# Kernel optimization log

Measured on AMD Instinct MI355X. Metric: run time of the kernel, lower is better.

Reference implementation:

```python
import jax, jax.numpy as jnp
import numpy as np

VOCAB = 100000
EMB = 256
HID = 512
HH = HID // 2  # per-direction hidden
NTAGS = 12
START = 10
STOP = 11
SEQ = 2048
NEG = -10000.0


def setup_inputs() -> dict:
    key = jax.random.key(0)
    ks = jax.random.split(key, 18)
    s = 0.05
    inp = {
        "sentence": jax.random.randint(ks[0], (SEQ,), 0, VOCAB, dtype=jnp.int64 if jax.config.jax_enable_x64 else jnp.int32),
        "tags": jax.random.randint(ks[1], (SEQ,), 0, 10, dtype=jnp.int64 if jax.config.jax_enable_x64 else jnp.int32),
        "embed": jax.random.normal(ks[2], (VOCAB, EMB), jnp.float32) * s,
        "Wih_f": jax.random.normal(ks[3], (4 * HH, EMB), jnp.float32) * s,
        "Whh_f": jax.random.normal(ks[4], (4 * HH, HH), jnp.float32) * s,
        "bih_f": jax.random.normal(ks[5], (4 * HH,), jnp.float32) * s,
        "bhh_f": jax.random.normal(ks[6], (4 * HH,), jnp.float32) * s,
        "Wih_b": jax.random.normal(ks[7], (4 * HH, EMB), jnp.float32) * s,
        "Whh_b": jax.random.normal(ks[8], (4 * HH, HH), jnp.float32) * s,
        "bih_b": jax.random.normal(ks[9], (4 * HH,), jnp.float32) * s,
        "bhh_b": jax.random.normal(ks[10], (4 * HH,), jnp.float32) * s,
        "W_out": jax.random.normal(ks[11], (NTAGS, HID), jnp.float32) * s,
        "b_out": jax.random.normal(ks[12], (NTAGS,), jnp.float32) * s,
        "h0": jax.random.normal(ks[14], (2, HH), jnp.float32),
        "c0": jax.random.normal(ks[15], (2, HH), jnp.float32),
    }
    trans = jax.random.normal(ks[13], (NTAGS, NTAGS), jnp.float32)
    trans = trans.at[START, :].set(NEG)  # never transition INTO start
    trans = trans.at[:, STOP].set(NEG)   # never transition FROM stop
    inp["transitions"] = trans
    return inp


def _lstm_dir(x, h0, c0, Wih, Whh, bih, bhh):
    # x: [T, E]; PyTorch gate order i, f, g, o
    pre = x @ Wih.T + bih + bhh  # [T, 4*HH] precomputed input projection
    def step(carry, p):
        h, c = carry
        g = p + Whh @ h
        i, f, gg, o = jnp.split(g, 4)
        i = jax.nn.sigmoid(i)
        f = jax.nn.sigmoid(f)
        gg = jnp.tanh(gg)
        o = jax.nn.sigmoid(o)
        c = f * c + i * gg
        h = o * jnp.tanh(c)
        return (h, c), h
    _, hs = jax.lax.scan(step, (h0, c0), pre)
    return hs  # [T, HH]


def _forward_impl(sentence, tags, embed, Wih_f, Whh_f, bih_f, bhh_f,
                  Wih_b, Whh_b, bih_b, bhh_b, W_out, b_out, transitions, h0, c0):
    x = embed[sentence]  # [T, E]
    hf = _lstm_dir(x, h0[0], c0[0], Wih_f, Whh_f, bih_f, bhh_f)
    hb = jnp.flip(_lstm_dir(jnp.flip(x, 0), h0[1], c0[1], Wih_b, Whh_b, bih_b, bhh_b), 0)
    feats = jnp.concatenate([hf, hb], axis=-1) @ W_out.T + b_out  # [T, NTAGS]

    # CRF forward algorithm: log-semiring scan over time
    fv0 = jnp.full((NTAGS,), NEG, feats.dtype).at[START].set(0.0)
    def crf_step(fv, emit):
        # transitions[next, prev]; logsumexp over prev
        fv = jax.nn.logsumexp(fv[None, :] + transitions + emit[:, None], axis=1)
        return fv, None
    fv, _ = jax.lax.scan(crf_step, fv0, feats)
    forward_score = jax.nn.logsumexp(fv + transitions[STOP])

    # gold path score
    prev = jnp.concatenate([jnp.array([START], dtype=tags.dtype), tags[:-1]])
    emit_gold = jnp.take_along_axis(feats, tags[:, None], axis=1)[:, 0]
    gold_score = jnp.sum(transitions[tags, prev]) + jnp.sum(emit_gold) + transitions[STOP, tags[-1]]

    return forward_score - gold_score


def reference(sentence, tags, embed, Wih_f, Whh_f, bih_f, bhh_f,
              Wih_b, Whh_b, bih_b, bhh_b, W_out, b_out, transitions, h0, c0):
    return _forward_impl(sentence, tags, embed, Wih_f, Whh_f, bih_f, bhh_f,
                         Wih_b, Whh_b, bih_b, bhh_b, W_out, b_out, transitions, h0, c0)
```

## Files before the change

kernel.cpp:

```cpp
#include <hip/hip_runtime.h>
#include <hip/hip_bf16.h>
#include <stdint.h>

#define SEQ   2048
#define EMB   256
#define HHD   256
#define GATES 1024
#define NTAGS 12
#define START 10
#define STOP  11
#define CCH   16
#define CLEN  128

__device__ __forceinline__ int sdot4(uint32_t a, uint32_t b, int c) {
#if __has_builtin(__builtin_amdgcn_sdot4)
  return __builtin_amdgcn_sdot4((int)a, (int)b, c, false);
#else
  int r = c;
#pragma unroll
  for (int i = 0; i < 4; i++) {
    int av = (int)(signed char)((a >> (8 * i)) & 255);
    int bv = (int)(signed char)((b >> (8 * i)) & 255);
    r += av * bv;
  }
  return r;
#endif
}

__device__ __forceinline__ float fsig(float x) {
  float e = __expf(-x);
  return __builtin_amdgcn_rcpf(1.0f + e);
}

__device__ __forceinline__ int dpp_xor1(int x) {
  return __builtin_amdgcn_update_dpp(0, x, 0xB1, 0xF, 0xF, true);
}
__device__ __forceinline__ int dpp_xor2(int x) {
  return __builtin_amdgcn_update_dpp(0, x, 0x4E, 0xF, 0xF, true);
}
__device__ __forceinline__ float dpp_xor2_f(float x) {
  int r = __builtin_amdgcn_update_dpp(0, __float_as_int(x), 0x4E, 0xF, 0xF, true);
  return __int_as_float(r);
}

__global__ __launch_bounds__(256) void k_front(const float* __restrict__ whh_f,
                                               const float* __restrict__ whh_b,
                                               uint32_t* __restrict__ q4,
                                               float* __restrict__ scales,
                                               const int* __restrict__ sentence,
                                               const float* __restrict__ embed,
                                               const float* __restrict__ Wih_f,
                                               const float* __restrict__ bih_f,
                                               const float* __restrict__ bhh_f,
                                               const float* __restrict__ Wih_b,
                                               const float* __restrict__ bih_b,
                                               const float* __restrict__ bhh_b,
                                               float* __restrict__ pre) {
  if (blockIdx.x < 512) {
    const int row  = (blockIdx.x * 256 + threadIdx.x) >> 6;
    const int lane = threadIdx.x & 63;
    const int d = row >> 10, r = row & 1023;
    const float4 w = *(const float4*)((d ? whh_b : whh_f) + (long)r * HHD + lane * 4);
    float m = fmaxf(fmaxf(fabsf(w.x), fabsf(w.y)), fmaxf(fabsf(w.z), fabsf(w.w)));
#pragma unroll
    for (int off = 32; off; off >>= 1) m = fmaxf(m, __shfl_xor(m, off, 64));
    m = fmaxf(m, 1e-20f);
    const float inv = 127.f / m;
    int a = (int)rintf(w.x * inv), b = (int)rintf(w.y * inv);
    int c = (int)rintf(w.z * inv), e = (int)rintf(w.w * inv);
    q4[row * 64 + lane] = (uint32_t)(a & 255) | ((uint32_t)(b & 255) << 8) |
                          ((uint32_t)(c & 255) << 16) | ((uint32_t)(e & 255) << 24);
    if (lane == 0) scales[row] = m / 127.f;
    return;
  }
  const int bid2 = blockIdx.x - 512;
  const int dir  = bid2 >> 8;
  const int t0   = (bid2 & 255) * 8;
  const float* Wih = dir ? Wih_b : Wih_f;
  const float* bih = dir ? bih_b : bih_f;
  const float* bhh = dir ? bhh_b : bhh_f;

  __shared__ float xs[8][256];
  const int uu = threadIdx.x;
#pragma unroll
  for (int i = 0; i < 8; i++) {
    int s = sentence[t0 + i];
    xs[i][uu] = embed[(long)s * EMB + uu];
  }
  __syncthreads();

  float acc[4][8];
#pragma unroll
  for (int j = 0; j < 4; j++)
#pragma unroll
    for (int t = 0; t < 8; t++) acc[j][t] = 0.f;

  const float4* W4 = (const float4*)Wih;
  for (int kq = 0; kq < 64; kq++) {
    float4 w[4];
#pragma unroll
    for (int j = 0; j < 4; j++) w[j] = W4[(j * 256 + uu) * 64 + kq];
#pragma unroll
    for (int t = 0; t < 8; t++) {
      float4 xv = ((const float4*)xs[t])[kq];
#pragma unroll
      for (int j = 0; j < 4; j++)
        acc[j][t] += w[j].x * xv.x + w[j].y * xv.y + w[j].z * xv.z + w[j].w * xv.w;
    }
  }
  float bs[4];
#pragma unroll
  for (int j = 0; j < 4; j++) bs[j] = bih[j * 256 + uu] + bhh[j * 256 + uu];
#pragma unroll
  for (int t = 0; t < 8; t++) {
    float4 o = {acc[0][t] + bs[0], acc[1][t] + bs[1],
                acc[2][t] + bs[2], acc[3][t] + bs[3]};
    *(float4*)&pre[(((long)(dir * SEQ + t0 + t)) * HHD + uu) * 4] = o;
  }
}

__global__ __launch_bounds__(512, 2) void k_lstm(const uint32_t* __restrict__ q4,
                                                 const float* __restrict__ scales,
                                                 const float* __restrict__ pre,
                                                 const float* __restrict__ h0,
                                                 const float* __restrict__ c0,
                                                 float* __restrict__ hs) {
  const int dir  = blockIdx.x;
  const int L    = threadIdx.x;
  const int q    = L & 3;
  const int g    = L >> 2;
  const int p    = q & 1;
  const int half = q >> 1;
  const int u    = 2 * g + p;

  __shared__ __align__(16) uint8_t hbuf[2][256];

  const long base = (long)dir * GATES;

  uint4 wa[4][4], wb[4][4];
  const uint4* qq = (const uint4*)q4;
#pragma unroll
  for (int j = 0; j < 4; j++) {
    const int qj = q ^ j;
    const int rA = (2 * (qj >> 1)) * 256 + 2 * g + (qj & 1);
    const int rB = rA + 256;
#pragma unroll
    for (int k = 0; k < 4; k++) {
      wa[j][k] = qq[(base + rA) * 16 + 4 * q + k];
      wb[j][k] = qq[(base + rB) * 16 + 4 * q + k];
    }
  }
  const int rown = (2 * half) * 256 + u;
  const float sA = scales[base + rown];
  const float sB = scales[base + rown + 256];

  if (L < 256) {
    float v = h0[dir * HHD + L] * (127.f / 4.f);
    v = fminf(fmaxf(v, -127.f), 127.f);
    hbuf[0][L] = (uint8_t)(int)rintf(v);
  }
  float c_st = c0[dir * HHD + u];
  __syncthreads();

  const int t0 = dir ? (SEQ - 1) : 0;
  const long pstep = dir ? -(long)(HHD * 4) : (long)(HHD * 4);
  const long hstep = dir ? -(long)HHD : (long)HHD;
  const float* pp = pre + (long)dir * SEQ * (HHD * 4) + ((long)t0 * HHD + u) * 4 + 2 * half;
  float* hp       = hs  + (long)dir * SEQ * HHD + (long)t0 * HHD + u;
  const float gmul = half ? 2.f : 1.f;
  const int write_h = ((L & 2) == 0);

  for (int s = 0; s < SEQ; s++) {
    const float2 pr = *(const float2*)pp;

    const uint4* hq4 = (const uint4*)(hbuf[s & 1] + (q << 6));
    const uint4 h0v = hq4[0], h1v = hq4[1], h2v = hq4[2], h3v = hq4[3];

    int pa0 = 0, pa1 = 0, pa2 = 0, pa3 = 0;
    int pb0 = 0, pb1 = 0, pb2 = 0, pb3 = 0;
#pragma unroll
    for (int k = 0; k < 4; k++) {
      const uint4 hk = (k == 0) ? h0v : (k == 1) ? h1v : (k == 2) ? h2v : h3v;
      pa0 = sdot4(wa[0][k].x, hk.x, pa0); pa0 = sdot4(wa[0][k].y, hk.y, pa0);
      pa0 = sdot4(wa[0][k].z, hk.z, pa0); pa0 = sdot4(wa[0][k].w, hk.w, pa0);
      pa1 = sdot4(wa[1][k].x, hk.x, pa1); pa1 = sdot4(wa[1][k].y, hk.y, pa1);
      pa1 = sdot4(wa[1][k].z, hk.z, pa1); pa1 = sdot4(wa[1][k].w, hk.w, pa1);
      pa2 = sdot4(wa[2][k].x, hk.x, pa2); pa2 = sdot4(wa[2][k].y, hk.y, pa2);
      pa2 = sdot4(wa[2][k].z, hk.z, pa2); pa2 = sdot4(wa[2][k].w, hk.w, pa2);
      pa3 = sdot4(wa[3][k].x, hk.x, pa3); pa3 = sdot4(wa[3][k].y, hk.y, pa3);
      pa3 = sdot4(wa[3][k].z, hk.z, pa3); pa3 = sdot4(wa[3][k].w, hk.w, pa3);
      pb0 = sdot4(wb[0][k].x, hk.x, pb0); pb0 = sdot4(wb[0][k].y, hk.y, pb0);
      pb0 = sdot4(wb[0][k].z, hk.z, pb0); pb0 = sdot4(wb[0][k].w, hk.w, pb0);
      pb1 = sdot4(wb[1][k].x, hk.x, pb1); pb1 = sdot4(wb[1][k].y, hk.y, pb1);
      pb1 = sdot4(wb[1][k].z, hk.z, pb1); pb1 = sdot4(wb[1][k].w, hk.w, pb1);
      pb2 = sdot4(wb[2][k].x, hk.x, pb2); pb2 = sdot4(wb[2][k].y, hk.y, pb2);
      pb2 = sdot4(wb[2][k].z, hk.z, pb2); pb2 = sdot4(wb[2][k].w, hk.w, pb2);
      pb3 = sdot4(wb[3][k].x, hk.x, pb3); pb3 = sdot4(wb[3][k].y, hk.y, pb3);
      pb3 = sdot4(wb[3][k].z, hk.z, pb3); pb3 = sdot4(wb[3][k].w, hk.w, pb3);
    }
    const int tA = pa0 + dpp_xor1(pa1);
    const int tA2 = pa2 + dpp_xor1(pa3);
    const int sumA = tA + dpp_xor2(tA2);
    const int tB = pb0 + dpp_xor1(pb1);
    const int tB2 = pb2 + dpp_xor1(pb3);
    const int sumB = tB + dpp_xor2(tB2);

    const float hsc = (s == 0) ? (4.f / 127.f) : (1.f / 127.f);
    const float gA = pr.x + sA * hsc * (float)sumA;
    const float gB = pr.y + sB * hsc * (float)sumB;

    const float v0 = fsig(gA * gmul) * gmul - (gmul - 1.f);
    const float v1 = fsig(gB);
    const float p0 = dpp_xor2_f(v0);
    const float p1 = dpp_xor2_f(v1);
    const float iv = half ? p0 : v0;
    const float fv = half ? p1 : v1;
    const float gv = half ? v0 : p0;
    const float ov = half ? v1 : p1;

    c_st = fv * c_st + iv * gv;
    const float hv = ov * (2.f * fsig(2.f * c_st) - 1.f);

    if (write_h) {
      *hp = hv;
      hbuf[(s + 1) & 1][u] = (uint8_t)(int)rintf(hv * 127.f);
    }
    pp += pstep;
    hp += hstep;
    __syncthreads();
  }
}

__global__ __launch_bounds__(192) void k_feats(const float* __restrict__ hs,
                                               const float* __restrict__ W_out,
                                               const float* __restrict__ b_out,
                                               float* __restrict__ feats) {
  __shared__ float Wl[12 * 520];
  const int tid = threadIdx.x;
  for (int i = tid; i < 12 * 512; i += 192) Wl[(i / 512) * 520 + (i % 512)] = W_out[i];
  __syncthreads();

  const int tl = tid / 12, n = tid % 12;
  const int t = blockIdx.x * 16 + tl;
  const float4* hf4 = (const float4*)(hs + (long)t * HHD);
  const float4* hb4 = (const float4*)(hs + (long)SEQ * HHD + (long)t * HHD);
  const float4* Wa  = (const float4*)&Wl[n * 520];
  const float4* Wb  = (const float4*)&Wl[n * 520 + 256];

  float acc = b_out[n];
#pragma unroll 8
  for (int j = 0; j < 64; j++) {
    float4 w = Wa[j], h = hf4[j];
    acc += w.x * h.x + w.y * h.y + w.z * h.z + w.w * h.w;
  }
#pragma unroll 8
  for (int j = 0; j < 64; j++) {
    float4 w = Wb[j], h = hb4[j];
    acc += w.x * h.x + w.y * h.y + w.z * h.z + w.w * h.w;
  }
  feats[t * NTAGS + n] = acc;
}

__global__ __launch_bounds__(192) void k_crf_chunk(const float* __restrict__ feats,
                                                   const float* __restrict__ trans,
                                                   float* __restrict__ Pc) {
  const int ch  = blockIdx.x;
  const int tid = threadIdx.x;
  const int n   = tid & 15;
  const int p   = tid >> 4;
  const int nn  = (n < 12) ? n : 11;

  __shared__ float fe[CLEN * NTAGS];
  for (int i = tid; i < CLEN * NTAGS; i += 192) fe[i] = feats[ch * CLEN * NTAGS + i];
  __syncthreads();

  float trn[12];
#pragma unroll
  for (int j = 0; j < 12; j++) trn[j] = trans[nn * 12 + j];

  float Mv = trans[nn * 12 + p] + fe[nn];
  for (int t = 1; t < CLEN; t++) {
    float x[12], m = -1e30f;
#pragma unroll
    for (int j = 0; j < 12; j++) {
      x[j] = trn[j] + __shfl(Mv, (tid & 48) | j, 64);
      m = fmaxf(m, x[j]);
    }
    float ss = 0.f;
#pragma unroll
    for (int j = 0; j < 12; j++) ss += __expf(x[j] - m);
    Mv = fe[t * NTAGS + nn] + m + __logf(ss);
  }
  if (n < 12) Pc[ch * 144 + n * 12 + p] = Mv;
}

__global__ __launch_bounds__(128) void k_crf_final(const float* __restrict__ Pc,
                                                   const float* __restrict__ feats,
                                                   const int* __restrict__ tags,
                                                   const float* __restrict__ trans,
                                                   float* __restrict__ out) {
  __shared__ float Pl[CCH * 144];
  __shared__ float res[2];
  const int tid = threadIdx.x;
  for (int i = tid; i < CCH * 144; i += 128) Pl[i] = Pc[i];
  __syncthreads();

  if (tid < 64) {
    const int n  = tid;
    const int nn = (n < 12) ? n : 11;
    float fv = (n == START) ? 0.f : -10000.f;
    for (int c = 0; c < CCH; c++) {
      float x[12], m = -1e30f;
#pragma unroll
      for (int j = 0; j < 12; j++) {
        x[j] = Pl[c * 144 + nn * 12 + j] + __shfl(fv, j, 64);
        m = fmaxf(m, x[j]);
      }
      float ss = 0.f;
#pragma unroll
      for (int j = 0; j < 12; j++) ss += __expf(x[j] - m);
      fv = m + __logf(ss);
    }
    const float v = fv + trans[STOP * 12 + nn];
    float xs[12], m = -1e30f;
#pragma unroll
    for (int j = 0; j < 12; j++) {
      xs[j] = __shfl(v, j, 64);
      m = fmaxf(m, xs[j]);
    }
    float ss = 0.f;
#pragma unroll
    for (int j = 0; j < 12; j++) ss += __expf(xs[j] - m);
    if (tid == 0) res[0] = m + __logf(ss);
  } else {
    const int i = tid - 64;
    float gp = 0.f;
    for (int b = 0; b < 32; b++) {
      int t  = b * 64 + i;
      int tg = tags[t];
      int pv = (t == 0) ? START : tags[t - 1];
      gp += trans[tg * 12 + pv] + feats[t * NTAGS + tg];
    }
#pragma unroll
    for (int off = 32; off; off >>= 1) gp += __shfl_xor(gp, off, 64);
    if (i == 0) res[1] = gp + trans[STOP * 12 + tags[SEQ - 1]];
  }
  __syncthreads();
  if (tid == 0) out[0] = res[0] - res[1];
}

extern "C" void kernel_launch(void* const* d_in, const int* in_sizes, int n_in,
                              void* d_out, int out_size, void* d_ws, size_t ws_size,
                              hipStream_t stream) {
  const int*   sentence = (const int*)  d_in[0];
  const int*   tags     = (const int*)  d_in[1];
  const float* embed    = (const float*)d_in[2];
  const float* Wih_f    = (const float*)d_in[3];
  const float* Whh_f    = (const float*)d_in[4];
  const float* bih_f    = (const float*)d_in[5];
  const float* bhh_f    = (const float*)d_in[6];
  const float* Wih_b    = (const float*)d_in[7];
  const float* Whh_b    = (const float*)d_in[8];
  const float* bih_b    = (const float*)d_in[9];
  const float* bhh_b    = (const float*)d_in[10];
  const float* W_out    = (const float*)d_in[11];
  const float* b_out    = (const float*)d_in[12];
  const float* h0       = (const float*)d_in[13];
  const float* c0       = (const float*)d_in[14];
  const float* trans    = (const float*)d_in[15];
  float* out = (float*)d_out;

  char* ws = (char*)d_ws;
  uint32_t* q4    = (uint32_t*)ws;
  float*    scales= (float*)(ws + (512l << 10));
  float*    pre   = (float*)(ws + (1l  << 20));
  float*    hs    = (float*)(ws + (17l << 20));
  float*    feats = (float*)(ws + (21l << 20));
  float*    Pc    = (float*)(ws + (21l << 20) + (128l<<10));

  k_front<<<1024, 256, 0, stream>>>(Whh_f, Whh_b, q4, scales,
                                    sentence, embed, Wih_f, bih_f, bhh_f,
                                    Wih_b, bih_b, bhh_b, pre);
  k_lstm<<<2, 512, 0, stream>>>(q4, scales, pre, h0, c0, hs);
  k_feats<<<128, 192, 0, stream>>>(hs, W_out, b_out, feats);
  k_crf_chunk<<<CCH, 192, 0, stream>>>(feats, trans, Pc);
  k_crf_final<<<1, 128, 0, stream>>>(Pc, feats, tags, trans, out);
}
```

Measured before the change: 1.821 ms.

## Fuse emission projection into CRF chunk kernel and reorder input-projection loop

Merges the feats projection kernel into the CRF chunk kernel, so each of the 16 blocks computes its 128 timesteps of emissions into shared memory and then runs the chunked log-semiring scan. This removes one launch and the global round trip of feats before the scan. The price is lower parallelism: 16 blocks of 1024 threads replace 128 blocks for the projection. Separately, the input-projection loop in the front kernel now iterates gates outermost, so each thread streams one weight row at a time instead of four interleaved rows. That reorder changes the access pattern and cuts register pressure but rereads the shared x vectors four times.

```diff
diff --git a/kernel.cpp b/kernel.cpp
--- a/kernel.cpp
+++ b/kernel.cpp
@@ -96,16 +96,16 @@
     for (int t = 0; t < 8; t++) acc[j][t] = 0.f;
 
   const float4* W4 = (const float4*)Wih;
-  for (int kq = 0; kq < 64; kq++) {
-    float4 w[4];
-#pragma unroll
-    for (int j = 0; j < 4; j++) w[j] = W4[(j * 256 + uu) * 64 + kq];
-#pragma unroll
-    for (int t = 0; t < 8; t++) {
-      float4 xv = ((const float4*)xs[t])[kq];
-#pragma unroll
-      for (int j = 0; j < 4; j++)
-        acc[j][t] += w[j].x * xv.x + w[j].y * xv.y + w[j].z * xv.z + w[j].w * xv.w;
+#pragma unroll
+  for (int j = 0; j < 4; j++) {
+    const float4* Wrow = W4 + (long)(j * 256 + uu) * 64;
+    for (int kq = 0; kq < 64; kq++) {
+      const float4 w = Wrow[kq];
+#pragma unroll
+      for (int t = 0; t < 8; t++) {
+        const float4 xv = ((const float4*)xs[t])[kq];
+        acc[j][t] += w.x * xv.x + w.y * xv.y + w.z * xv.z + w.w * xv.w;
+      }
     }
   }
   float bs[4];
@@ -231,67 +231,67 @@
   }
 }
 
-__global__ __launch_bounds__(192) void k_feats(const float* __restrict__ hs,
+__global__ __launch_bounds__(1024) void k_tail(const float* __restrict__ hs,
                                                const float* __restrict__ W_out,
                                                const float* __restrict__ b_out,
-                                               float* __restrict__ feats) {
-  __shared__ float Wl[12 * 520];
-  const int tid = threadIdx.x;
-  for (int i = tid; i < 12 * 512; i += 192) Wl[(i / 512) * 520 + (i % 512)] = W_out[i];
-  __syncthreads();
-
-  const int tl = tid / 12, n = tid % 12;
-  const int t = blockIdx.x * 16 + tl;
-  const float4* hf4 = (const float4*)(hs + (long)t * HHD);
-  const float4* hb4 = (const float4*)(hs + (long)SEQ * HHD + (long)t * HHD);
-  const float4* Wa  = (const float4*)&Wl[n * 520];
-  const float4* Wb  = (const float4*)&Wl[n * 520 + 256];
-
-  float acc = b_out[n];
-#pragma unroll 8
-  for (int j = 0; j < 64; j++) {
-    float4 w = Wa[j], h = hf4[j];
-    acc += w.x * h.x + w.y * h.y + w.z * h.z + w.w * h.w;
-  }
-#pragma unroll 8
-  for (int j = 0; j < 64; j++) {
-    float4 w = Wb[j], h = hb4[j];
-    acc += w.x * h.x + w.y * h.y + w.z * h.z + w.w * h.w;
-  }
-  feats[t * NTAGS + n] = acc;
-}
-
-__global__ __launch_bounds__(192) void k_crf_chunk(const float* __restrict__ feats,
-                                                   const float* __restrict__ trans,
-                                                   float* __restrict__ Pc) {
+                                               const float* __restrict__ trans,
+                                               float* __restrict__ feats,
+                                               float* __restrict__ Pc) {
   const int ch  = blockIdx.x;
   const int tid = threadIdx.x;
-  const int n   = tid & 15;
-  const int p   = tid >> 4;
-  const int nn  = (n < 12) ? n : 11;
-
+
+  __shared__ float Wl[12 * 520];
   __shared__ float fe[CLEN * NTAGS];
-  for (int i = tid; i < CLEN * NTAGS; i += 192) fe[i] = feats[ch * CLEN * NTAGS + i];
-  __syncthreads();
-
-  float trn[12];
-#pragma unroll
-  for (int j = 0; j < 12; j++) trn[j] = trans[nn * 12 + j];
-
-  float Mv = trans[nn * 12 + p] + fe[nn];
-  for (int t = 1; t < CLEN; t++) {
-    float x[12], m = -1e30f;
-#pragma unroll
-    for (int j = 0; j < 12; j++) {
-      x[j] = trn[j] + __shfl(Mv, (tid & 48) | j, 64);
-      m = fmaxf(m, x[j]);
-    }
-    float ss = 0.f;
-#pragma unroll
-    for (int j = 0; j < 12; j++) ss += __expf(x[j] - m);
-    Mv = fe[t * NTAGS + nn] + m + __logf(ss);
-  }
-  if (n < 12) Pc[ch * 144 + n * 12 + p] = Mv;
+  for (int i = tid; i < 12 * 512; i += 1024) Wl[(i / 512) * 520 + (i % 512)] = W_out[i];
+  __syncthreads();
+
+  for (int idx = tid; idx < CLEN * NTAGS; idx += 1024) {
+    const int tl = idx / 12, n = idx % 12;
+    const int t  = ch * CLEN + tl;
+    const float4* hf4 = (const float4*)(hs + (long)t * HHD);
+    const float4* hb4 = (const float4*)(hs + (long)SEQ * HHD + (long)t * HHD);
+    const float4* Wa  = (const float4*)&Wl[n * 520];
+    const float4* Wb  = (const float4*)&Wl[n * 520 + 256];
+    float acc = b_out[n];
+#pragma unroll 8
+    for (int j = 0; j < 64; j++) {
+      float4 w = Wa[j], h = hf4[j];
+      acc += w.x * h.x + w.y * h.y + w.z * h.z + w.w * h.w;
+    }
+#pragma unroll 8
+    for (int j = 0; j < 64; j++) {
+      float4 w = Wb[j], h = hb4[j];
+      acc += w.x * h.x + w.y * h.y + w.z * h.z + w.w * h.w;
+    }
+    fe[tl * NTAGS + n] = acc;
+    feats[t * NTAGS + n] = acc;
+  }
+  __syncthreads();
+
+  if (tid < 192) {
+    const int n   = tid & 15;
+    const int p   = tid >> 4;
+    const int nn  = (n < 12) ? n : 11;
+
+    float trn[12];
+#pragma unroll
+    for (int j = 0; j < 12; j++) trn[j] = trans[nn * 12 + j];
+
+    float Mv = trn[p] + fe[nn];
+    for (int t = 1; t < CLEN; t++) {
+      float x[12], m = -1e30f;
+#pragma unroll
+      for (int j = 0; j < 12; j++) {
+        x[j] = trn[j] + __shfl(Mv, (tid & 48) | j, 64);
+        m = fmaxf(m, x[j]);
+      }
+      float ss = 0.f;
+#pragma unroll
+      for (int j = 0; j < 12; j++) ss += __expf(x[j] - m);
+      Mv = fe[t * NTAGS + nn] + m + __logf(ss);
+    }
+    if (n < 12) Pc[ch * 144 + n * 12 + p] = Mv;
+  }
 }
 
 __global__ __launch_bounds__(128) void k_crf_final(const float* __restrict__ Pc,
@@ -382,7 +382,6 @@
                                     sentence, embed, Wih_f, bih_f, bhh_f,
                                     Wih_b, bih_b, bhh_b, pre);
   k_lstm<<<2, 512, 0, stream>>>(q4, scales, pre, h0, c0, hs);
-  k_feats<<<128, 192, 0, stream>>>(hs, W_out, b_out, feats);
-  k_crf_chunk<<<CCH, 192, 0, stream>>>(feats, trans, Pc);
+  k_tail<<<CCH, 1024, 0, stream>>>(hs, W_out, b_out, trans, feats, Pc);
   k_crf_final<<<1, 128, 0, stream>>>(Pc, feats, tags, trans, out);
 }
```

Result: no change. 1.798 ms (-1.3%).
